# Optimization experiments

Measured on AMD Instinct MI355X. Metric: run time of the kernel, lower is better.

Reference implementation:

```python
import jax, jax.numpy as jnp
import numpy as np

B, K, D = 32768, 4096, 256


def setup_inputs() -> dict:
    key = jax.random.key(0)
    k1, k2 = jax.random.split(key)
    z_e_x = jax.random.normal(k1, (B, D), dtype=jnp.float32)
    # embedding.weight initialized N(0, 1) per init='normal'
    weight = jax.random.normal(k2, (K, D), dtype=jnp.float32)
    return {"z_e_x": z_e_x, "weight": weight}


def reference(z_e_x, weight):
    # Squared L2 distances ||z - e||^2 = ||z||^2 - 2 z.e + ||e||^2,
    # computed via a GEMM instead of materializing the [B, K, D] broadcast
    # that the torch code builds with repeat(). Same math as
    # sum((z_e_x_ - codebook_vectors)**2, dim=-1).
    z_sq = jnp.sum(z_e_x * z_e_x, axis=-1, keepdims=True)          # [B, 1]
    e_sq = jnp.sum(weight * weight, axis=-1)                        # [K]
    cross = jnp.einsum('bd,kd->bk', z_e_x, weight)                  # [B, K]
    distances = z_sq - 2.0 * cross + e_sq                           # [B, K]
    # greedy=True path of forward()
    index = jnp.argmin(distances, axis=-1)                          # [B] int
    # straight_through(): quantized lookup + straight-through estimator
    z_q_x = weight[index]                                           # [B, D]
    sg_z_e_x = z_e_x + jax.lax.stop_gradient(z_q_x - z_e_x)         # [B, D]
    return (sg_z_e_x, z_q_x, index)
```

## Files before the change

### kernel.cpp

```cpp
#include <hip/hip_runtime.h>

typedef _Float16 half8 __attribute__((ext_vector_type(8)));
typedef _Float16 half4 __attribute__((ext_vector_type(4)));
typedef float floatx16 __attribute__((ext_vector_type(16)));

constexpr int Bn = 32768, Kn = 4096, Dn = 256;
constexpr int BM = 128;
constexpr int NI = 64;
constexpr int NCH = 256;

__global__ void prep_kernel(const float* __restrict__ w, float* __restrict__ esq,
                            char* __restrict__ w16) {
    int code = blockIdx.x * 4 + (threadIdx.x >> 6);
    int l = threadIdx.x & 63;
    float4 v = *reinterpret_cast<const float4*>(w + (size_t)code * Dn + l * 4);
    float s = v.x * v.x + v.y * v.y + v.z * v.z + v.w * v.w;
    #pragma unroll
    for (int off = 32; off; off >>= 1) s += __shfl_xor(s, off);
    if (l == 0) esq[code] = s;

    float fv[4] = {v.x, v.y, v.z, v.w};
    half4 h, lo;
    #pragma unroll
    for (int j = 0; j < 4; ++j) {
        _Float16 hh = (_Float16)fv[j];
        h[j] = hh;
        lo[j] = (_Float16)(fv[j] - (float)hh);
    }
    const int kc = l >> 4;
    const int o_h = (l & 15) * 8;
    const int swz = (code & 15) << 4;
    char* row = w16 + (size_t)code * 1024 + kc * 256;
    *reinterpret_cast<half4*>(row + (o_h ^ swz)) = h;
    *reinterpret_cast<half4*>(row + ((o_h + 128) ^ swz)) = lo;
}

#define GLDS(gsrc, ldsoff)                                                        \
    __builtin_amdgcn_global_load_lds(                                             \
        (const __attribute__((address_space(1))) unsigned int*)(const void*)(gsrc),\
        (__attribute__((address_space(3))) unsigned int*)(void*)(smem + (ldsoff)), \
        16, 0, 0)

#define MFMA(a, b, c) __builtin_amdgcn_mfma_f32_32x32x16_f16((a), (b), (c), 0, 0, 0)

__global__ void
__launch_bounds__(512, 2)
vq_kernel(const float* __restrict__ z, const float* __restrict__ w,
          const float* __restrict__ esq, const char* __restrict__ w16,
          float* __restrict__ out0, float* __restrict__ out1,
          float* __restrict__ out2) {
    __shared__ char smem[84480];
    const int tid = threadIdx.x;
    const int wv = tid >> 6, l = tid & 63;
    const int mw = wv >> 1, nw = wv & 1;
    const int lh = l >> 5, ll = l & 31;
    const int blkRow = blockIdx.x * BM;

    float* esq_s = reinterpret_cast<float*>(smem + 65536);
    #pragma unroll
    for (int j = 0; j < 8; ++j) esq_s[j * 512 + tid] = esq[j * 512 + tid];

    half8 a_hi[16], a_lo[16];
    {
        const float* zr = z + (size_t)(blkRow + mw * 32 + ll) * Dn + lh * 8;
        #pragma unroll
        for (int ks = 0; ks < 16; ++ks) {
            float4 f0 = *reinterpret_cast<const float4*>(zr + ks * 16);
            float4 f1 = *reinterpret_cast<const float4*>(zr + ks * 16 + 4);
            float fv[8] = {f0.x, f0.y, f0.z, f0.w, f1.x, f1.y, f1.z, f1.w};
            #pragma unroll
            for (int j = 0; j < 8; ++j) {
                _Float16 h = (_Float16)fv[j];
                a_hi[ks][j] = h;
                a_lo[ks][j] = (_Float16)(fv[j] - (float)h);
            }
        }
    }

    const size_t srcOff0 = (size_t)(wv * 8 + (l >> 4)) * 1024 + (l & 15) * 16;
    const int ldsOff0 = wv * 2048;

    int addrH[4], addrL[4];
    {
        const int c_loc = nw * 32 + ll;
        const int swz = (c_loc & 15) << 4;
        #pragma unroll
        for (int ks = 0; ks < 4; ++ks) {
            const int o = ks * 32 + lh * 16;
            addrH[ks] = c_loc * 256 + (o ^ swz);
            addrL[ks] = c_loc * 256 + ((o + 128) ^ swz);
        }
    }

    float rbv[16];
    unsigned rbn[4] = {0, 0, 0, 0};
    #pragma unroll
    for (int q = 0; q < 16; ++q) rbv[q] = 3.4e38f;

    asm volatile("s_waitcnt vmcnt(0)" ::: "memory");
    __syncthreads();

    GLDS(w16 + srcOff0, ldsOff0);
    GLDS(w16 + 4096 + srcOff0, ldsOff0 + 1024);
    GLDS(w16 + 256 + srcOff0, 16384 + ldsOff0);
    GLDS(w16 + 256 + 4096 + srcOff0, 16384 + ldsOff0 + 1024);
    asm volatile("s_waitcnt vmcnt(2)" ::: "memory");
    __builtin_amdgcn_s_barrier();
    asm volatile("" ::: "memory");

    half8 sh0[4], sl0[4], sh1[4], sl1[4];
    #pragma unroll
    for (int ks = 0; ks < 4; ++ks) {
        sh0[ks] = *reinterpret_cast<const half8*>(smem + addrH[ks]);
        sl0[ks] = *reinterpret_cast<const half8*>(smem + addrL[ks]);
    }

    for (int ni = 0; ni < NI; ++ni) {
        floatx16 accA = {}, accB = {};
        #pragma unroll
        for (int kc = 0; kc < 4; ++kc) {
            const int c = ni * 4 + kc;
            if (c + 2 < NCH) {
                const char* s2 = w16 + (size_t)((c + 2) >> 2) * 65536 + ((c + 2) & 3) * 256 + srcOff0;
                const int d2 = (((kc + 2) & 3) * 16384) + ldsOff0;
                GLDS(s2, d2);
                GLDS(s2 + 4096, d2 + 1024);
                asm volatile("s_waitcnt vmcnt(2)" ::: "memory");
            } else {
                asm volatile("s_waitcnt vmcnt(0)" ::: "memory");
            }
            __builtin_amdgcn_s_barrier();
            asm volatile("" ::: "memory");
            const char* nb = smem + ((kc + 1) & 3) * 16384;
            if (kc & 1) {
                if (c + 1 < NCH) {
                    #pragma unroll
                    for (int ks = 0; ks < 4; ++ks) {
                        sh0[ks] = *reinterpret_cast<const half8*>(nb + addrH[ks]);
                        sl0[ks] = *reinterpret_cast<const half8*>(nb + addrL[ks]);
                    }
                }
                __builtin_amdgcn_s_setprio(1);
                #pragma unroll
                for (int ks = 0; ks < 4; ++ks) {
                    const int ksg = kc * 4 + ks;
                    accA = MFMA(a_hi[ksg], sh1[ks], accA);
                    accB = MFMA(a_hi[ksg], sl1[ks], accB);
                    accB = MFMA(a_lo[ksg], sh1[ks], accB);
                }
                __builtin_amdgcn_s_setprio(0);
            } else {
                if (c + 1 < NCH) {
                    #pragma unroll
                    for (int ks = 0; ks < 4; ++ks) {
                        sh1[ks] = *reinterpret_cast<const half8*>(nb + addrH[ks]);
                        sl1[ks] = *reinterpret_cast<const half8*>(nb + addrL[ks]);
                    }
                }
                __builtin_amdgcn_s_setprio(1);
                #pragma unroll
                for (int ks = 0; ks < 4; ++ks) {
                    const int ksg = kc * 4 + ks;
                    accA = MFMA(a_hi[ksg], sh0[ks], accA);
                    accB = MFMA(a_hi[ksg], sl0[ks], accB);
                    accB = MFMA(a_lo[ksg], sh0[ks], accB);
                }
                __builtin_amdgcn_s_setprio(0);
            }
        }
        const float e = esq_s[ni * 64 + nw * 32 + ll];
        #pragma unroll
        for (int q = 0; q < 16; ++q) {
            const float v = fmaf(-2.f, accA[q], fmaf(-2.f, accB[q], e));
            const int sh = (q & 3) * 8;
            if (v < rbv[q]) {
                rbv[q] = v;
                rbn[q >> 2] = (rbn[q >> 2] & ~(255u << sh)) | ((unsigned)ni << sh);
            }
        }
    }

    int2* comb = reinterpret_cast<int2*>(smem + 81920);
    #pragma unroll
    for (int q = 0; q < 16; ++q) {
        float v = rbv[q];
        int i = (int)((rbn[q >> 2] >> ((q & 3) * 8)) & 255u) * 64 + nw * 32 + ll;
        #pragma unroll
        for (int off = 1; off < 32; off <<= 1) {
            float ov = __shfl_xor(v, off);
            int oi = __shfl_xor(i, off);
            if (ov < v || (ov == v && oi < i)) { v = ov; i = oi; }
        }
        if (ll == 0) {
            const int r32 = (q & 3) + 8 * (q >> 2) + 4 * lh;
            comb[(mw * 32 + r32) * 2 + nw] = make_int2(__float_as_int(v), i);
        }
    }
    __syncthreads();
    int* idxF = reinterpret_cast<int*>(smem + 83968);
    if (tid < 128) {
        int2 c0 = comb[tid * 2], c1 = comb[tid * 2 + 1];
        float v0 = __int_as_float(c0.x), v1 = __int_as_float(c1.x);
        idxF[tid] = (v1 < v0 || (v1 == v0 && c1.y < c0.y)) ? c1.y : c0.y;
    }
    __syncthreads();

    {
        const int r = tid >> 2, p4 = tid & 3;
        const int gRow = blkRow + r;
        const int idx = idxF[r];
        const float* wr = w + (size_t)idx * Dn + p4 * 64;
        const float* zr = z + (size_t)gRow * Dn + p4 * 64;
        float* o0 = out0 + (size_t)gRow * Dn + p4 * 64;
        float* o1 = out1 + (size_t)gRow * Dn + p4 * 64;
        #pragma unroll
        for (int q = 0; q < 16; ++q) {
            float4 wq = *reinterpret_cast<const float4*>(wr + q * 4);
            float4 zq = *reinterpret_cast<const float4*>(zr + q * 4);
            *reinterpret_cast<float4*>(o1 + q * 4) = wq;
            float4 sg;
            sg.x = zq.x + (wq.x - zq.x);
            sg.y = zq.y + (wq.y - zq.y);
            sg.z = zq.z + (wq.z - zq.z);
            sg.w = zq.w + (wq.w - zq.w);
            *reinterpret_cast<float4*>(o0 + q * 4) = sg;
        }
        if (p4 == 0) out2[gRow] = (float)idx;
    }
}

extern "C" void kernel_launch(void* const* d_in, const int* in_sizes, int n_in,
                              void* d_out, int out_size, void* d_ws, size_t ws_size,
                              hipStream_t stream) {
    (void)in_sizes; (void)n_in; (void)out_size; (void)ws_size;
    const float* z = (const float*)d_in[0];
    const float* w = (const float*)d_in[1];
    float* esq = (float*)d_ws;
    char* w16 = (char*)d_ws + 16384;
    float* out0 = (float*)d_out;
    float* out1 = out0 + (size_t)Bn * Dn;
    float* out2 = out1 + (size_t)Bn * Dn;

    prep_kernel<<<Kn / 4, 256, 0, stream>>>(w, esq, w16);
    vq_kernel<<<Bn / BM, 512, 0, stream>>>(z, w, esq, w16, out0, out1, out2);
}
```

Measured before the change: 325.6 us.

## Halve block rows, use triple-buffered LDS ring with fully unrolled phase macro

```diff
diff --git a/kernel.cpp b/kernel.cpp
--- a/kernel.cpp
+++ b/kernel.cpp
@@ -5,8 +5,7 @@
 typedef float floatx16 __attribute__((ext_vector_type(16)));
 
 constexpr int Bn = 32768, Kn = 4096, Dn = 256;
-constexpr int BM = 128;
-constexpr int NI = 64;
+constexpr int BM = 64;
 constexpr int NCH = 256;
 
 __global__ void prep_kernel(const float* __restrict__ w, float* __restrict__ esq,
@@ -43,22 +42,88 @@
 
 #define MFMA(a, b, c) __builtin_amdgcn_mfma_f32_32x32x16_f16((a), (b), (c), 0, 0, 0)
 
+#define PHASE(CB, J, DO_DMA, DO_READ) do {                                         \
+    constexpr int KC = (J) & 3, B3 = (J) % 3, PAR = (J) & 1;                       \
+    const int c_ = (CB) + (J);                                                     \
+    if (KC == 0) { accA = vzero; accB = vzero; }                                   \
+    asm volatile("s_waitcnt vmcnt(0)" ::: "memory");                               \
+    __builtin_amdgcn_s_barrier();                                                  \
+    asm volatile("" ::: "memory");                                                 \
+    if (DO_DMA) {                                                                  \
+        const char* s2 = w16 + (size_t)((c_ + 2) >> 2) * 65536 +                   \
+                         ((c_ + 2) & 3) * 256 + srcOff0;                           \
+        constexpr int BW = ((B3) + 2) % 3;                                         \
+        const int d2 = BW * 16384 + dmaDst0;                                       \
+        GLDS(s2, d2); GLDS(s2 + 4096, d2 + 1024);                                  \
+        GLDS(s2 + 8192, d2 + 2048); GLDS(s2 + 12288, d2 + 3072);                   \
+    }                                                                              \
+    if (DO_READ) {       \
+        const char* nb = smem + (((B3) + 1) % 3) * 16384;                          \
+        if (PAR == 0) {                                                            \
+            _Pragma("unroll")                                                      \
+            for (int ks = 0; ks < 4; ++ks) {                                       \
+                sh1[ks] = *reinterpret_cast<const half8*>(nb + addrH[ks]);         \
+                sl1[ks] = *reinterpret_cast<const half8*>(nb + addrL[ks]);         \
+            }                                                                      \
+        } else {                                                                   \
+            _Pragma("unroll")                                                      \
+            for (int ks = 0; ks < 4; ++ks) {                                       \
+                sh0[ks] = *reinterpret_cast<const half8*>(nb + addrH[ks]);         \
+                sl0[ks] = *reinterpret_cast<const half8*>(nb + addrL[ks]);         \
+            }                                                                      \
+        }                                                                          \
+    }                                                                              \
+    __builtin_amdgcn_s_setprio(1);                                                 \
+    _Pragma("unroll")                                                              \
+    for (int ks = 0; ks < 4; ++ks) {            \
+        constexpr int KB = KC * 4;                                                 \
+        if (PAR == 0) {                                                            \
+            accA = MFMA(a_hi[KB + ks], sh0[ks], accA);                             \
+            accB = MFMA(a_hi[KB + ks], sl0[ks], accB);                             \
+            accB = MFMA(a_lo[KB + ks], sh0[ks], accB);                             \
+        } else {                                                                   \
+            accA = MFMA(a_hi[KB + ks], sh1[ks], accA);                             \
+            accB = MFMA(a_hi[KB + ks], sl1[ks], accB);                             \
+            accB = MFMA(a_lo[KB + ks], sh1[ks], accB);                             \
+        }                                                                          \
+    }                                                                              \
+    __builtin_amdgcn_s_setprio(0);                                                 \
+    if (KC == 3) {     \
+        const int tile_ = c_ >> 2;                                                 \
+        const float e = esqf[tile_ * 64 + nw * 32 + ll];                           \
+        _Pragma("unroll")                                                          \
+        for (int q = 0; q < 16; ++q) {                                             \
+            const float v = fmaf(-2.f, accA[q], fmaf(-2.f, accB[q], e));           \
+            const int sh = (q & 3) * 8;                                            \
+            if (v < rbv[q]) {                                                      \
+                rbv[q] = v;                                                        \
+                rbn[q >> 2] = (rbn[q >> 2] & ~(255u << sh)) |                      \
+                              ((unsigned)tile_ << sh);                             \
+            }                                                                      \
+        }                                                                          \
+    }                                                                              \
+} while (0)
+
 __global__ void
-__launch_bounds__(512, 2)
+__launch_bounds__(256, 2)
 vq_kernel(const float* __restrict__ z, const float* __restrict__ w,
           const float* __restrict__ esq, const char* __restrict__ w16,
           float* __restrict__ out0, float* __restrict__ out1,
           float* __restrict__ out2) {
-    __shared__ char smem[84480];
+    __shared__ char smem[66816];
     const int tid = threadIdx.x;
     const int wv = tid >> 6, l = tid & 63;
     const int mw = wv >> 1, nw = wv & 1;
     const int lh = l >> 5, ll = l & 31;
     const int blkRow = blockIdx.x * BM;
 
-    float* esq_s = reinterpret_cast<float*>(smem + 65536);
-    #pragma unroll
-    for (int j = 0; j < 8; ++j) esq_s[j * 512 + tid] = esq[j * 512 + tid];
+    float* esqf = reinterpret_cast<float*>(smem + 49152);
+    {
+        float4* es4 = reinterpret_cast<float4*>(esqf);
+        const float4* eg4 = reinterpret_cast<const float4*>(esq);
+        #pragma unroll
+        for (int j = 0; j < 4; ++j) es4[j * 256 + tid] = eg4[j * 256 + tid];
+    }
 
     half8 a_hi[16], a_lo[16];
     {
@@ -77,8 +142,8 @@
         }
     }
 
-    const size_t srcOff0 = (size_t)(wv * 8 + (l >> 4)) * 1024 + (l & 15) * 16;
-    const int ldsOff0 = wv * 2048;
+    const size_t srcOff0 = (size_t)(wv * 16 + (l >> 4)) * 1024 + (l & 15) * 16;
+    const int dmaDst0 = wv * 4096;
 
     int addrH[4], addrL[4];
     {
@@ -92,95 +157,47 @@
         }
     }
 
+    const floatx16 vzero = {};
+    floatx16 accA = vzero, accB = vzero;
     float rbv[16];
     unsigned rbn[4] = {0, 0, 0, 0};
     #pragma unroll
     for (int q = 0; q < 16; ++q) rbv[q] = 3.4e38f;
 
+    half8 sh0[4], sl0[4], sh1[4], sl1[4];
+
     asm volatile("s_waitcnt vmcnt(0)" ::: "memory");
     __syncthreads();
 
-    GLDS(w16 + srcOff0, ldsOff0);
-    GLDS(w16 + 4096 + srcOff0, ldsOff0 + 1024);
-    GLDS(w16 + 256 + srcOff0, 16384 + ldsOff0);
-    GLDS(w16 + 256 + 4096 + srcOff0, 16384 + ldsOff0 + 1024);
-    asm volatile("s_waitcnt vmcnt(2)" ::: "memory");
+    GLDS(w16 + srcOff0, dmaDst0);
+    GLDS(w16 + 4096 + srcOff0, dmaDst0 + 1024);
+    GLDS(w16 + 8192 + srcOff0, dmaDst0 + 2048);
+    GLDS(w16 + 12288 + srcOff0, dmaDst0 + 3072);
+    GLDS(w16 + 256 + srcOff0, 16384 + dmaDst0);
+    GLDS(w16 + 256 + 4096 + srcOff0, 16384 + dmaDst0 + 1024);
+    GLDS(w16 + 256 + 8192 + srcOff0, 16384 + dmaDst0 + 2048);
+    GLDS(w16 + 256 + 12288 + srcOff0, 16384 + dmaDst0 + 3072);
+    asm volatile("s_waitcnt vmcnt(0)" ::: "memory");
     __builtin_amdgcn_s_barrier();
     asm volatile("" ::: "memory");
-
-    half8 sh0[4], sl0[4], sh1[4], sl1[4];
     #pragma unroll
     for (int ks = 0; ks < 4; ++ks) {
         sh0[ks] = *reinterpret_cast<const half8*>(smem + addrH[ks]);
         sl0[ks] = *reinterpret_cast<const half8*>(smem + addrL[ks]);
     }
 
-    for (int ni = 0; ni < NI; ++ni) {
-        floatx16 accA = {}, accB = {};
-        #pragma unroll
-        for (int kc = 0; kc < 4; ++kc) {
-            const int c = ni * 4 + kc;
-            if (c + 2 < NCH) {
-                const char* s2 = w16 + (size_t)((c + 2) >> 2) * 65536 + ((c + 2) & 3) * 256 + srcOff0;
-                const int d2 = (((kc + 2) & 3) * 16384) + ldsOff0;
-                GLDS(s2, d2);
-                GLDS(s2 + 4096, d2 + 1024);
-                asm volatile("s_waitcnt vmcnt(2)" ::: "memory");
-            } else {
-                asm volatile("s_waitcnt vmcnt(0)" ::: "memory");
-            }
-            __builtin_amdgcn_s_barrier();
-            asm volatile("" ::: "memory");
-            const char* nb = smem + ((kc + 1) & 3) * 16384;
-            if (kc & 1) {
-                if (c + 1 < NCH) {
-                    #pragma unroll
-                    for (int ks = 0; ks < 4; ++ks) {
-                        sh0[ks] = *reinterpret_cast<const half8*>(nb + addrH[ks]);
-                        sl0[ks] = *reinterpret_cast<const half8*>(nb + addrL[ks]);
-                    }
-                }
-                __builtin_amdgcn_s_setprio(1);
-                #pragma unroll
-                for (int ks = 0; ks < 4; ++ks) {
-                    const int ksg = kc * 4 + ks;
-                    accA = MFMA(a_hi[ksg], sh1[ks], accA);
-                    accB = MFMA(a_hi[ksg], sl1[ks], accB);
-                    accB = MFMA(a_lo[ksg], sh1[ks], accB);
-                }
-                __builtin_amdgcn_s_setprio(0);
-            } else {
-                if (c + 1 < NCH) {
-                    #pragma unroll
-                    for (int ks = 0; ks < 4; ++ks) {
-                        sh1[ks] = *reinterpret_cast<const half8*>(nb + addrH[ks]);
-                        sl1[ks] = *reinterpret_cast<const half8*>(nb + addrL[ks]);
-                    }
-                }
-                __builtin_amdgcn_s_setprio(1);
-                #pragma unroll
-                for (int ks = 0; ks < 4; ++ks) {
-                    const int ksg = kc * 4 + ks;
-                    accA = MFMA(a_hi[ksg], sh0[ks], accA);
-                    accB = MFMA(a_hi[ksg], sl0[ks], accB);
-                    accB = MFMA(a_lo[ksg], sh0[ks], accB);
-                }
-                __builtin_amdgcn_s_setprio(0);
-            }
-        }
-        const float e = esq_s[ni * 64 + nw * 32 + ll];
-        #pragma unroll
-        for (int q = 0; q < 16; ++q) {
-            const float v = fmaf(-2.f, accA[q], fmaf(-2.f, accB[q], e));
-            const int sh = (q & 3) * 8;
-            if (v < rbv[q]) {
-                rbv[q] = v;
-                rbn[q >> 2] = (rbn[q >> 2] & ~(255u << sh)) | ((unsigned)ni << sh);
-            }
-        }
-    }
-
-    int2* comb = reinterpret_cast<int2*>(smem + 81920);
+    for (int cb = 0; cb < 252; cb += 12) {
+        PHASE(cb, 0, 1, 1);  PHASE(cb, 1, 1, 1);  PHASE(cb, 2, 1, 1);
+        PHASE(cb, 3, 1, 1);  PHASE(cb, 4, 1, 1);  PHASE(cb, 5, 1, 1);
+        PHASE(cb, 6, 1, 1);  PHASE(cb, 7, 1, 1);  PHASE(cb, 8, 1, 1);
+        PHASE(cb, 9, 1, 1);  PHASE(cb, 10, 1, 1); PHASE(cb, 11, 1, 1);
+    }
+    PHASE(252, 0, 1, 1);
+    PHASE(252, 1, 1, 1);
+    PHASE(252, 2, 0, 1);
+    PHASE(252, 3, 0, 0);
+
+    int2* comb = reinterpret_cast<int2*>(smem + 65536);
     #pragma unroll
     for (int q = 0; q < 16; ++q) {
         float v = rbv[q];
@@ -197,8 +214,8 @@
         }
     }
     __syncthreads();
-    int* idxF = reinterpret_cast<int*>(smem + 83968);
-    if (tid < 128) {
+    int* idxF = reinterpret_cast<int*>(smem + 66560);
+    if (tid < 64) {
         int2 c0 = comb[tid * 2], c1 = comb[tid * 2 + 1];
         float v0 = __int_as_float(c0.x), v1 = __int_as_float(c1.x);
         idxF[tid] = (v1 < v0 || (v1 == v0 && c1.y < c0.y)) ? c1.y : c0.y;
@@ -242,5 +259,5 @@
     float* out2 = out1 + (size_t)Bn * Dn;
 
     prep_kernel<<<Kn / 4, 256, 0, stream>>>(w, esq, w16);
-    vq_kernel<<<Bn / BM, 512, 0, stream>>>(z, w, esq, w16, out0, out1, out2);
+    vq_kernel<<<Bn / BM, 256, 0, stream>>>(z, w, esq, w16, out0, out1, out2);
 }
```

Measured after the change: 640.2 us. +96.6%, slower.
